# Kernel tuning notes

Hardware: AMD Instinct MI355X
Metric: run time of the kernel (lower is better)

The kernel has to match this reference:

```python
import jax, jax.numpy as jnp
import numpy as np

VOCAB = 32000
HIDDEN = 1024
BATCH = 4
SEQ = 2048


def setup_inputs() -> dict:
    key = jax.random.key(0)
    k_ids, k_w, k_b = jax.random.split(key, 3)
    input_ids = jax.random.randint(k_ids, (BATCH, SEQ), 0, VOCAB, dtype=jnp.int64 if jax.config.jax_enable_x64 else jnp.int32)
    # torch nn.Linear(vocab, hidden): weight [hidden, vocab], bias [hidden]
    W = jax.random.normal(k_w, (HIDDEN, VOCAB), dtype=jnp.float32) * (1.0 / np.sqrt(VOCAB))
    b = jax.random.normal(k_b, (HIDDEN,), dtype=jnp.float32) * 0.02
    return {"input_ids": input_ids, "W": W, "b": b}


def reference(input_ids, W, b):
    # Faithful to the original: one-hot the ids then run the dense Linear.
    # E: [B, S, V] one-hot float, out = E @ W^T + b -> [B, S, H]
    E = jax.nn.one_hot(input_ids, VOCAB, dtype=jnp.float32)
    X = jnp.einsum("bsv,hv->bsh", E, W) + b
    return X
```

## Files before the change

kernel.cpp:

```cpp
#include <hip/hip_runtime.h>


#define VOCAB   32000
#define HIDDEN  1024
#define CBIN    256
#define NBIN    125
#define ROWS    64
#define NCH     (HIDDEN/ROWS)
#define CHUNK   1024
#define NCHK    8
#define NTOK    8192

__device__ __forceinline__ unsigned short f2bf(float f) {
    unsigned u = __float_as_uint(f);
    return (unsigned short)((u + 0x7FFFu + ((u >> 16) & 1u)) >> 16);
}
__device__ __forceinline__ float bf2f(unsigned short h) {
    return __uint_as_float((unsigned)h << 16);
}

__global__ __launch_bounds__(256, 4) void fused_onehot_kernel(
    const int* __restrict__ ids,
    const float* __restrict__ W,
    const float* __restrict__ b,
    float* __restrict__ out)
{
    const int bin = blockIdx.x;
    const int c0  = bin * CBIN;
    const int h0  = blockIdx.y * ROWS;
    const int t   = threadIdx.x;

    __shared__ unsigned short tile[ROWS * CBIN];
    __shared__ int m_s[CHUNK];
    __shared__ int cnt_s[NCHK];

    if (t < NCHK) cnt_s[t] = 0;

    const int c4 = (t & 63) * 4;
    const int r0 = t >> 6;
    #pragma unroll
    for (int batch = 0; batch < 2; ++batch) {
        float4 wv[8];
        #pragma unroll
        for (int i = 0; i < 8; ++i) {
            const int r = r0 + 4 * (batch * 8 + i);
            wv[i] = *reinterpret_cast<const float4*>(
                &W[(size_t)(h0 + r) * VOCAB + c0 + c4]);
        }
        #pragma unroll
        for (int i = 0; i < 8; ++i) {
            const int r  = r0 + 4 * (batch * 8 + i);
            const int cs = (c4 + (r & ~3)) & 255;
            const unsigned lo = (unsigned)f2bf(wv[i].x) | ((unsigned)f2bf(wv[i].y) << 16);
            const unsigned hi = (unsigned)f2bf(wv[i].z) | ((unsigned)f2bf(wv[i].w) << 16);
            *reinterpret_cast<uint2*>(&tile[r * CBIN + cs]) = make_uint2(lo, hi);
        }
    }
    __syncthreads();

    const int g  = t & 15;
    const int q  = t >> 4;
    const int r4 = g * 4;
    const float4 bv = *reinterpret_cast<const float4*>(&b[h0 + r4]);

    #pragma unroll
    for (int c = 0; c < NCHK; ++c) {
        if (c) __syncthreads();

        {
            const int4 v4 = reinterpret_cast<const int4*>(ids + c * CHUNK)[t];
            const int v[4] = {v4.x, v4.y, v4.z, v4.w};
            const int tb = c * CHUNK + t * 4;
            #pragma unroll
            for (int k = 0; k < 4; ++k) {
                const int d = v[k] - c0;
                if ((unsigned)d < CBIN) {
                    const int p = atomicAdd(&cnt_s[c], 1);
                    m_s[p] = ((tb + k) << 8) | d;
                }
            }
        }
        __syncthreads();

        const int cnt = cnt_s[c];
        for (int j = q; j < cnt; j += 16) {
            const int m   = m_s[j];
            const int tok = m >> 8;
            const int d   = m & 255;
            const int cs  = (d + r4) & 255;
            float4 o;
            o.x = bf2f(tile[(r4 + 0) * CBIN + cs]) + bv.x;
            o.y = bf2f(tile[(r4 + 1) * CBIN + cs]) + bv.y;
            o.z = bf2f(tile[(r4 + 2) * CBIN + cs]) + bv.z;
            o.w = bf2f(tile[(r4 + 3) * CBIN + cs]) + bv.w;
            *reinterpret_cast<float4*>(&out[(size_t)tok * HIDDEN + h0 + r4]) = o;
        }
    }
}

__global__ __launch_bounds__(256) void fallback_kernel(
    const int* __restrict__ ids, const float* __restrict__ W,
    const float* __restrict__ b, float* __restrict__ out, int n_tokens)
{
    const int t = threadIdx.x;
    const int sub = t >> 6, lane = t & 63;
    const int token = blockIdx.x * 4 + sub;
    if (token >= n_tokens) return;
    const int id = ids[token];
    const float* Wcol = W + (size_t)id;
    float v[16];
    #pragma unroll
    for (int j = 0; j < 4; ++j) {
        const int h0 = j * 256 + lane * 4;
        #pragma unroll
        for (int k = 0; k < 4; ++k)
            v[j * 4 + k] = Wcol[(size_t)(h0 + k) * VOCAB];
    }
    float* orow = out + (size_t)token * HIDDEN;
    #pragma unroll
    for (int j = 0; j < 4; ++j) {
        const int h0 = j * 256 + lane * 4;
        const float4 bv = *reinterpret_cast<const float4*>(&b[h0]);
        float4 o;
        o.x = v[j*4+0] + bv.x; o.y = v[j*4+1] + bv.y;
        o.z = v[j*4+2] + bv.z; o.w = v[j*4+3] + bv.w;
        *reinterpret_cast<float4*>(&orow[h0]) = o;
    }
}

extern "C" void kernel_launch(void* const* d_in, const int* in_sizes, int n_in,
                              void* d_out, int out_size, void* d_ws, size_t ws_size,
                              hipStream_t stream)
{
    const int*   ids = (const int*)d_in[0];
    const float* W   = (const float*)d_in[1];
    const float* b   = (const float*)d_in[2];
    float*       out = (float*)d_out;

    const int n_tokens = in_sizes[0];

    if (n_tokens == NTOK) {
        fused_onehot_kernel<<<dim3(NBIN, NCH), dim3(256), 0, stream>>>(
            ids, W, b, out);
    } else {
        fallback_kernel<<<dim3((n_tokens + 3) / 4), dim3(256), 0, stream>>>(
            ids, W, b, out, n_tokens);
    }
}
```

Before: 39.15 us.

## Process two 64-row W slabs per block, prefetching the second into registers

Each block now covers 128 hidden rows instead of 64 and halves the grid in y. The second 64-row slab of W is loaded into registers before the first scatter phase, so its global-memory latency overlaps the first slab's id-binning and output writes. The cost is roughly 64 extra float4 registers per thread, which may lower occupancy under the launch bound of 4. The ids are also scanned twice per block.

Result: faster. 37.19 us (-5.0%).

```diff
diff --git a/kernel.cpp b/kernel.cpp
--- a/kernel.cpp
+++ b/kernel.cpp
@@ -5,8 +5,9 @@
 #define HIDDEN  1024
 #define CBIN    256
 #define NBIN    125
-#define ROWS    64
-#define NCH     (HIDDEN/ROWS)
+#define HROWS   128
+#define SROWS   64
+#define NCH     (HIDDEN/HROWS)
 #define CHUNK   1024
 #define NCHK    8
 #define NTOK    8192
@@ -27,73 +28,127 @@
 {
     const int bin = blockIdx.x;
     const int c0  = bin * CBIN;
-    const int h0  = blockIdx.y * ROWS;
+    const int h0  = blockIdx.y * HROWS;
     const int t   = threadIdx.x;
 
-    __shared__ unsigned short tile[ROWS * CBIN];
+    __shared__ unsigned short tile[SROWS * CBIN];
     __shared__ int m_s[CHUNK];
-    __shared__ int cnt_s[NCHK];
-
-    if (t < NCHK) cnt_s[t] = 0;
+    __shared__ int cnt_s[2 * NCHK];
 
     const int c4 = (t & 63) * 4;
     const int r0 = t >> 6;
-    #pragma unroll
-    for (int batch = 0; batch < 2; ++batch) {
-        float4 wv[8];
-        #pragma unroll
-        for (int i = 0; i < 8; ++i) {
-            const int r = r0 + 4 * (batch * 8 + i);
-            wv[i] = *reinterpret_cast<const float4*>(
-                &W[(size_t)(h0 + r) * VOCAB + c0 + c4]);
-        }
-        #pragma unroll
-        for (int i = 0; i < 8; ++i) {
-            const int r  = r0 + 4 * (batch * 8 + i);
-            const int cs = (c4 + (r & ~3)) & 255;
-            const unsigned lo = (unsigned)f2bf(wv[i].x) | ((unsigned)f2bf(wv[i].y) << 16);
-            const unsigned hi = (unsigned)f2bf(wv[i].z) | ((unsigned)f2bf(wv[i].w) << 16);
-            *reinterpret_cast<uint2*>(&tile[r * CBIN + cs]) = make_uint2(lo, hi);
-        }
-    }
+
+    float4 wa[16];
+    #pragma unroll
+    for (int i = 0; i < 16; ++i) {
+        const int r = r0 + 4 * i;
+        wa[i] = *reinterpret_cast<const float4*>(
+            &W[(size_t)(h0 + r) * VOCAB + c0 + c4]);
+    }
+    if (t < 2 * NCHK) cnt_s[t] = 0;
+
+    #pragma unroll
+    for (int i = 0; i < 16; ++i) {
+        const int r  = r0 + 4 * i;
+        const int cs = (c4 + (r & ~3)) & 255;
+        const unsigned lo = (unsigned)f2bf(wa[i].x) | ((unsigned)f2bf(wa[i].y) << 16);
+        const unsigned hi = (unsigned)f2bf(wa[i].z) | ((unsigned)f2bf(wa[i].w) << 16);
+        *reinterpret_cast<uint2*>(&tile[r * CBIN + cs]) = make_uint2(lo, hi);
+    }
+
+    float4 wb[16];
+    #pragma unroll
+    for (int i = 0; i < 16; ++i) {
+        const int r = r0 + 4 * i;
+        wb[i] = *reinterpret_cast<const float4*>(
+            &W[(size_t)(h0 + SROWS + r) * VOCAB + c0 + c4]);
+    }
+    __builtin_amdgcn_sched_barrier(0);
+
     __syncthreads();
 
     const int g  = t & 15;
     const int q  = t >> 4;
     const int r4 = g * 4;
-    const float4 bv = *reinterpret_cast<const float4*>(&b[h0 + r4]);
-
-    #pragma unroll
-    for (int c = 0; c < NCHK; ++c) {
-        if (c) __syncthreads();
-
-        {
-            const int4 v4 = reinterpret_cast<const int4*>(ids + c * CHUNK)[t];
-            const int v[4] = {v4.x, v4.y, v4.z, v4.w};
-            const int tb = c * CHUNK + t * 4;
-            #pragma unroll
-            for (int k = 0; k < 4; ++k) {
-                const int d = v[k] - c0;
-                if ((unsigned)d < CBIN) {
-                    const int p = atomicAdd(&cnt_s[c], 1);
-                    m_s[p] = ((tb + k) << 8) | d;
+
+    {
+        const float4 bv = *reinterpret_cast<const float4*>(&b[h0 + r4]);
+        for (int c = 0; c < NCHK; ++c) {
+            if (c) __syncthreads();
+            {
+                const int4 v4 = reinterpret_cast<const int4*>(ids + c * CHUNK)[t];
+                const int v[4] = {v4.x, v4.y, v4.z, v4.w};
+                const int tb = c * CHUNK + t * 4;
+                #pragma unroll
+                for (int k = 0; k < 4; ++k) {
+                    const int d = v[k] - c0;
+                    if ((unsigned)d < CBIN) {
+                        const int p = atomicAdd(&cnt_s[c], 1);
+                        m_s[p] = ((tb + k) << 8) | d;
+                    }
                 }
             }
+            __syncthreads();
+            const int cnt = cnt_s[c];
+            for (int j = q; j < cnt; j += 16) {
+                const int m   = m_s[j];
+                const int tok = m >> 8;
+                const int d   = m & 255;
+                const int cs  = (d + r4) & 255;
+                float4 o;
+                o.x = bf2f(tile[(r4 + 0) * CBIN + cs]) + bv.x;
+                o.y = bf2f(tile[(r4 + 1) * CBIN + cs]) + bv.y;
+                o.z = bf2f(tile[(r4 + 2) * CBIN + cs]) + bv.z;
+                o.w = bf2f(tile[(r4 + 3) * CBIN + cs]) + bv.w;
+                *reinterpret_cast<float4*>(
+                    &out[(size_t)tok * HIDDEN + h0 + r4]) = o;
+            }
         }
-        __syncthreads();
-
-        const int cnt = cnt_s[c];
-        for (int j = q; j < cnt; j += 16) {
-            const int m   = m_s[j];
-            const int tok = m >> 8;
-            const int d   = m & 255;
-            const int cs  = (d + r4) & 255;
-            float4 o;
-            o.x = bf2f(tile[(r4 + 0) * CBIN + cs]) + bv.x;
-            o.y = bf2f(tile[(r4 + 1) * CBIN + cs]) + bv.y;
-            o.z = bf2f(tile[(r4 + 2) * CBIN + cs]) + bv.z;
-            o.w = bf2f(tile[(r4 + 3) * CBIN + cs]) + bv.w;
-            *reinterpret_cast<float4*>(&out[(size_t)tok * HIDDEN + h0 + r4]) = o;
+    }
+    __syncthreads();
+
+    #pragma unroll
+    for (int i = 0; i < 16; ++i) {
+        const int r  = r0 + 4 * i;
+        const int cs = (c4 + (r & ~3)) & 255;
+        const unsigned lo = (unsigned)f2bf(wb[i].x) | ((unsigned)f2bf(wb[i].y) << 16);
+        const unsigned hi = (unsigned)f2bf(wb[i].z) | ((unsigned)f2bf(wb[i].w) << 16);
+        *reinterpret_cast<uint2*>(&tile[r * CBIN + cs]) = make_uint2(lo, hi);
+    }
+    __syncthreads();
+
+    {
+        const float4 bv = *reinterpret_cast<const float4*>(&b[h0 + SROWS + r4]);
+        for (int c = 0; c < NCHK; ++c) {
+            if (c) __syncthreads();
+            {
+                const int4 v4 = reinterpret_cast<const int4*>(ids + c * CHUNK)[t];
+                const int v[4] = {v4.x, v4.y, v4.z, v4.w};
+                const int tb = c * CHUNK + t * 4;
+                #pragma unroll
+                for (int k = 0; k < 4; ++k) {
+                    const int d = v[k] - c0;
+                    if ((unsigned)d < CBIN) {
+                        const int p = atomicAdd(&cnt_s[NCHK + c], 1);
+                        m_s[p] = ((tb + k) << 8) | d;
+                    }
+                }
+            }
+            __syncthreads();
+            const int cnt = cnt_s[NCHK + c];
+            for (int j = q; j < cnt; j += 16) {
+                const int m   = m_s[j];
+                const int tok = m >> 8;
+                const int d   = m & 255;
+                const int cs  = (d + r4) & 255;
+                float4 o;
+                o.x = bf2f(tile[(r4 + 0) * CBIN + cs]) + bv.x;
+                o.y = bf2f(tile[(r4 + 1) * CBIN + cs]) + bv.y;
+                o.z = bf2f(tile[(r4 + 2) * CBIN + cs]) + bv.z;
+                o.w = bf2f(tile[(r4 + 3) * CBIN + cs]) + bv.w;
+                *reinterpret_cast<float4*>(
+                    &out[(size_t)tok * HIDDEN + h0 + SROWS + r4]) = o;
+            }
         }
     }
 }
```
